# Performance work log

Measured on AMD Instinct MI355X. Metric: run time of the kernel, lower is better.

## Reference

```python
import jax, jax.numpy as jnp
import numpy as np

N, NF1, NF2, NH, OUT, K = 16384, 2000, 10000, 512, 16, 19
BN_EPS = 1e-5

def _bn(x, g, b, m, v):
    # eval-mode BatchNorm1d with running stats
    return (x - m) * jax.lax.rsqrt(v + BN_EPS) * g + b


def setup_inputs() -> dict:
    key = jax.random.key(0)
    ks = jax.random.split(key, 24)
    f32 = jnp.float32
    def w(k, shape):
        return jax.random.normal(k, shape, f32) * 0.02
    inp = {
        "rna": jax.random.normal(ks[0], (N, NF1), f32),
        "atac": jax.random.normal(ks[1], (N, NF2), f32),
        "index_rna": jnp.arange(N, dtype=jnp.int32),
        "index_atac": jnp.arange(N, dtype=jnp.int32),
        "eps": jax.random.normal(ks[2], (N, OUT), f32),
        # RNA encoder
        "W_r1": w(ks[3], (NH, NF1)), "b_r1": jnp.zeros((NH,), f32),
        "g_r": jnp.ones((NH,), f32), "be_r": jnp.zeros((NH,), f32),
        "m_r": jnp.zeros((NH,), f32), "v_r": jnp.ones((NH,), f32),
        "W_rmu": w(ks[4], (OUT, NH)), "b_rmu": jnp.zeros((OUT,), f32),
        "W_rvar": w(ks[5], (OUT, NH)), "b_rvar": jnp.zeros((OUT,), f32),
        # ATAC encoder
        "W_a1": w(ks[6], (NH, NF2)), "b_a1": jnp.zeros((NH,), f32),
        "g_a": jnp.ones((NH,), f32), "be_a": jnp.zeros((NH,), f32),
        "m_a": jnp.zeros((NH,), f32), "v_a": jnp.ones((NH,), f32),
        "W_amu": w(ks[7], (OUT, NH)), "b_amu": jnp.zeros((OUT,), f32),
        "W_avar": w(ks[8], (OUT, NH)), "b_avar": jnp.zeros((OUT,), f32),
        # decoder
        "W_d1": w(ks[9], (NH, OUT)), "b_d1": jnp.zeros((NH,), f32),
        "g_d": jnp.ones((NH,), f32), "be_d": jnp.zeros((NH,), f32),
        "m_d": jnp.zeros((NH,), f32), "v_d": jnp.ones((NH,), f32),
        "W_d4": w(ks[10], (NF1 + NF2, NH)), "b_d4": jnp.zeros((NF1 + NF2,), f32),
        "cluster": jax.random.normal(ks[11], (K, OUT), f32),
    }
    return inp


def reference(rna, atac, index_rna, index_atac, eps,
              W_r1, b_r1, g_r, be_r, m_r, v_r, W_rmu, b_rmu, W_rvar, b_rvar,
              W_a1, b_a1, g_a, be_a, m_a, v_a, W_amu, b_amu, W_avar, b_avar,
              W_d1, b_d1, g_d, be_d, m_d, v_d, W_d4, b_d4, cluster):
    n = rna.shape[0]
    # encoders (dropout is identity in eval mode)
    h_rna = jax.nn.relu(_bn(rna @ W_r1.T + b_r1, g_r, be_r, m_r, v_r))
    zm_rna = h_rna @ W_rmu.T + b_rmu
    zv_rna = jnp.exp(h_rna @ W_rvar.T + b_rvar)
    h_atac = jax.nn.relu(_bn(atac @ W_a1.T + b_a1, g_a, be_a, m_a, v_a))
    zm_atac = h_atac @ W_amu.T + b_amu
    zv_atac = jnp.exp(h_atac @ W_avar.T + b_avar)
    # vectorized scatter replacing the per-sample Python loop
    mu = jnp.ones((n, 2, OUT), rna.dtype)
    var = jnp.ones((n, 2, OUT), rna.dtype)
    mask = jnp.zeros((n, 2, OUT), rna.dtype)
    mu = mu.at[index_rna, 0].set(zm_rna).at[index_atac, 1].set(zm_atac)
    var = var.at[index_rna, 0].set(zv_rna).at[index_atac, 1].set(zv_atac)
    mask = mask.at[index_rna, 0].set(1.0).at[index_atac, 1].set(1.0)
    # product of experts over the modality axis (axis=1)
    T = mask / var
    T_sum = T.sum(axis=1) + 1.0            # [n, OUT]
    z_mu = (mu * T).sum(axis=1) / T_sum
    z_var = 1.0 / T_sum
    # Normal(z_mu, scale=z_var).rsample() with externally supplied eps
    z = z_mu + z_var * eps
    # student-t style soft assignment to clusters
    d2 = jnp.sum((z[:, None, :] - cluster[None, :, :]) ** 2, axis=2)  # [n, K]
    q = 1.0 / (1.0 + d2)
    q = q / q.sum(axis=1, keepdims=True)
    # decoder
    h = jax.nn.relu(_bn(z @ W_d1.T + b_d1, g_d, be_d, m_d, v_d))
    recon_x = h @ W_d4.T + b_d4
    return (recon_x, z_mu, z_var, z, q)
```

## Files before the change

### kernel.cpp

```cpp
#include <hip/hip_runtime.h>
#include <hip/hip_bf16.h>

#define NS    16384
#define NF1c  2000
#define NF2c  10000
#define NH    512
#define KC    19
#define NREC  12000
#define NRECP 12032

typedef short bf16x8 __attribute__((ext_vector_type(8)));
typedef float f32x4  __attribute__((ext_vector_type(4)));

__device__ __forceinline__ unsigned short f2bf(float x) {
    return __builtin_bit_cast(unsigned short, __hip_bfloat16(x));
}
__device__ __forceinline__ float bf2f(unsigned short h) {
    return __builtin_bit_cast(float, (unsigned int)h << 16);
}

__device__ __forceinline__ void sync_nodrain() {
    asm volatile("s_waitcnt lgkmcnt(0)" ::: "memory");
    __builtin_amdgcn_s_barrier();
    asm volatile("" ::: "memory");
}

template<int BK> __device__ __forceinline__ int swz(int r) {
    return (BK == 32) ? ((r >> 1) & 3) : (r & 7);
}

__device__ __forceinline__ void gload16(const unsigned short* g, unsigned short* l) {
    __builtin_amdgcn_global_load_lds(
        (const __attribute__((address_space(1))) void*)g,
        (__attribute__((address_space(3))) void*)l, 16, 0, 0);
}

__global__ void k_cvt(const float* __restrict__ s, unsigned short* __restrict__ d, int n4) {
    int i = blockIdx.x * blockDim.x + threadIdx.x;
    int st = gridDim.x * blockDim.x;
    for (; i < n4; i += st) {
        float4 f = ((const float4*)s)[i];
        ushort4 o;
        o.x = f2bf(f.x); o.y = f2bf(f.y); o.z = f2bf(f.z); o.w = f2bf(f.w);
        ((ushort4*)d)[i] = o;
    }
}

__global__ void k_cvt_pad(const float* __restrict__ s, unsigned short* __restrict__ d,
                          int K, int Rv, long nchunks) {
    long i = (long)blockIdx.x * blockDim.x + threadIdx.x;
    const long stp = (long)gridDim.x * blockDim.x;
    const int Kp8 = K / 8;
    for (; i < nchunks; i += stp) {
        const long row = i / Kp8;
        const int  col = (int)(i - row * Kp8) * 8;
        __align__(16) unsigned short u[8] = {0, 0, 0, 0, 0, 0, 0, 0};
        if (row < Rv) {
            const float* p = s + row * (long)K + col;
            float4 f0 = *(const float4*)p;
            float4 f1 = *(const float4*)(p + 4);
            u[0] = f2bf(f0.x); u[1] = f2bf(f0.y); u[2] = f2bf(f0.z); u[3] = f2bf(f0.w);
            u[4] = f2bf(f1.x); u[5] = f2bf(f1.y); u[6] = f2bf(f1.z); u[7] = f2bf(f1.w);
        }
        *(uint4*)(d + row * (long)K + col) = *(uint4*)u;
    }
}

__global__ void k_prep_st(const float* __restrict__ g, const float* __restrict__ be,
                          const float* __restrict__ m, const float* __restrict__ v,
                          const float* __restrict__ b1,
                          float* __restrict__ s, float* __restrict__ t, int n) {
    int i = blockIdx.x * blockDim.x + threadIdx.x;
    if (i < n) {
        float sc = g[i] * rsqrtf(v[i] + 1e-5f);
        s[i] = sc;
        t[i] = be[i] + (b1[i] - m[i]) * sc;
    }
}

__global__ void k_zero(float* __restrict__ p, int n) {
    int i = blockIdx.x * blockDim.x + threadIdx.x;
    if (i < n) p[i] = 0.f;
}

__global__ __launch_bounds__(256)
void k_gemm(const void* __restrict__ Aptr, const unsigned short* __restrict__ B,
            int K, int Nn, int ntn,
            const float* __restrict__ sc, const float* __restrict__ sh,
            unsigned short* __restrict__ Hout)
{
    constexpr int BK = 64;
    constexpr int JC = BK / 16;
    __shared__ __align__(16) unsigned short As[2][128 * BK];
    __shared__ __align__(16) unsigned short Bs[2][128 * BK];

    const int nwg = gridDim.x;
    const int q8  = nwg >> 3;
    const int L   = (blockIdx.x & 7) * q8 + (blockIdx.x >> 3);
    const int tn  = L % ntn, tm = L / ntn;

    const int tid  = threadIdx.x;
    const int wave = tid >> 6, lane = tid & 63;
    const int wr   = wave >> 1, wc = wave & 1;
    const int lo   = lane & 15, hi = lane >> 4;
    const int srow = tid >> 1, shalf = tid & 1;
    const long arow = (long)tm * 128 + srow;
    const int  brow = tn * 128 + srow;
    const bool bok  = (brow < Nn);

    const float*          Af = (const float*)Aptr + arow * (long)K;
    const unsigned short* Bp = B + (long)brow * K;

    f32x4 acc[4][4];
#pragma unroll
    for (int i = 0; i < 4; i++)
#pragma unroll
        for (int j = 0; j < 4; j++) acc[i][j] = (f32x4){0.f, 0.f, 0.f, 0.f};

    float4 rfa[BK / 8];
    uint4  rb[JC];

    auto issue = [&](int k0, bool tail) {
        const int kb = k0 + shalf * (BK / 2);
        if (!tail) {
#pragma unroll
            for (int q = 0; q < BK / 8; q++) rfa[q] = *(const float4*)(Af + kb + q * 4);
        } else {
#pragma unroll
            for (int q = 0; q < BK / 8; q++) {
                float4 f;
                f.x = (kb + q * 4 + 0 < K) ? Af[kb + q * 4 + 0] : 0.f;
                f.y = (kb + q * 4 + 1 < K) ? Af[kb + q * 4 + 1] : 0.f;
                f.z = (kb + q * 4 + 2 < K) ? Af[kb + q * 4 + 2] : 0.f;
                f.w = (kb + q * 4 + 3 < K) ? Af[kb + q * 4 + 3] : 0.f;
                rfa[q] = f;
            }
        }
#pragma unroll
        for (int j = 0; j < JC; j++) rb[j] = (uint4){0, 0, 0, 0};
        if (bok) {
            if (!tail) {
#pragma unroll
                for (int j = 0; j < JC; j++) rb[j] = *(const uint4*)(Bp + kb + j * 8);
            } else {
#pragma unroll
                for (int j = 0; j < JC; j++) {
                    __align__(16) unsigned short t8[8];
#pragma unroll
                    for (int e = 0; e < 8; e++)
                        t8[e] = (kb + j * 8 + e < K) ? Bp[kb + j * 8 + e] : (unsigned short)0;
                    rb[j] = *(uint4*)t8;
                }
            }
        }
    };

    auto write = [&](int buf) {
        char* Ap = (char*)As[buf];
        char* Bq = (char*)Bs[buf];
        const int rbase = srow * (2 * BK);
        const int sw = swz<BK>(srow);
#pragma unroll
        for (int j = 0; j < JC; j++) {
            const int c = shalf * JC + j;
            const int pos = rbase + ((c ^ sw) << 4);
            uint4 av;
            unsigned int* w32 = (unsigned int*)&av;
            const float* fp = (const float*)&rfa[2 * j];
#pragma unroll
            for (int e = 0; e < 4; e++) {
                unsigned int l16 = f2bf(fp[2 * e]);
                unsigned int h16 = f2bf(fp[2 * e + 1]);
                w32[e] = l16 | (h16 << 16);
            }
            *(uint4*)(Ap + pos) = av;
            *(uint4*)(Bq + pos) = rb[j];
        }
    };

    auto comp = [&](int buf) {
        const char* Ap = (const char*)As[buf];
        const char* Bq = (const char*)Bs[buf];
#pragma unroll
        for (int s = 0; s < BK / 32; s++) {
            bf16x8 af[4], bfv[4];
#pragma unroll
            for (int f = 0; f < 4; f++) {
                const int ar = wr * 64 + f * 16 + lo;
                af[f]  = *(const bf16x8*)(Ap + ar * (2 * BK) + (((s * 4 + hi) ^ swz<BK>(ar)) << 4));
                const int br = wc * 64 + f * 16 + lo;
                bfv[f] = *(const bf16x8*)(Bq + br * (2 * BK) + (((s * 4 + hi) ^ swz<BK>(br)) << 4));
            }
#pragma unroll
            for (int i = 0; i < 4; i++)
#pragma unroll
                for (int j = 0; j < 4; j++)
                    acc[i][j] = __builtin_amdgcn_mfma_f32_16x16x32_bf16(af[i], bfv[j], acc[i][j], 0, 0, 0);
        }
    };

    const int ntf = K / BK;
    const bool rem = (K % BK) != 0;
    const int nt = ntf + (rem ? 1 : 0);
    issue(0, rem && nt == 1);
    for (int t = 0; t < nt; ++t) {
        write(t & 1);
        if (t + 1 < nt) issue((t + 1) * BK, rem && (t + 1 == nt - 1));
        sync_nodrain();
        comp(t & 1);
    }

#pragma unroll
    for (int i = 0; i < 4; i++) {
#pragma unroll
        for (int j = 0; j < 4; j++) {
            const int col = tn * 128 + wc * 64 + j * 16 + lo;
#pragma unroll
            for (int r = 0; r < 4; r++) {
                const long row = (long)tm * 128 + wr * 64 + i * 16 + hi * 4 + r;
                float v = fmaxf(acc[i][j][r] * sc[col] + sh[col], 0.f);
                Hout[row * NH + col] = f2bf(v);
            }
        }
    }
}

__global__ __launch_bounds__(256)
void k_rec(const unsigned short* __restrict__ A, const unsigned short* __restrict__ B,
           const float* __restrict__ bias, float* __restrict__ Fout)
{
    __shared__ __align__(16) unsigned short As[2][128 * 32];
    __shared__ __align__(16) unsigned short Bs[2][128 * 32];

    const int q8 = gridDim.x >> 3;
    const int L  = (blockIdx.x & 7) * q8 + (blockIdx.x >> 3);
    const int tn = L % 94, tm = L / 94;

    const int tid  = threadIdx.x;
    const int wave = tid >> 6, lane = tid & 63;
    const int wr = wave >> 1, wc = wave & 1;
    const int lo = lane & 15, hi = lane >> 4;

    const int rloc = lane >> 2, cch = lane & 3;
    const int row0 = wave * 32 + rloc;
    const int row1 = wave * 32 + 16 + rloc;
    const unsigned short* Ad0 = A + (long)(tm * 128 + row0) * NH + (cch ^ swz<32>(row0)) * 8;
    const unsigned short* Ad1 = A + (long)(tm * 128 + row1) * NH + (cch ^ swz<32>(row1)) * 8;
    const unsigned short* Bd0 = B + (long)(tn * 128 + row0) * NH + (cch ^ swz<32>(row0)) * 8;
    const unsigned short* Bd1 = B + (long)(tn * 128 + row1) * NH + (cch ^ swz<32>(row1)) * 8;

    f32x4 acc[4][4];
#pragma unroll
    for (int i = 0; i < 4; i++)
#pragma unroll
        for (int j = 0; j < 4; j++) acc[i][j] = (f32x4){0.f, 0.f, 0.f, 0.f};

    auto issue = [&](int buf) {
        gload16(Ad0, &As[buf][wave * 1024]);
        gload16(Ad1, &As[buf][wave * 1024 + 512]);
        gload16(Bd0, &Bs[buf][wave * 1024]);
        gload16(Bd1, &Bs[buf][wave * 1024 + 512]);
        Ad0 += 32; Ad1 += 32; Bd0 += 32; Bd1 += 32;
    };
    auto comp = [&](int buf) {
        const char* Ap = (const char*)As[buf];
        const char* Bq = (const char*)Bs[buf];
        bf16x8 af[4], bfv[4];
#pragma unroll
        for (int f = 0; f < 4; f++) {
            const int ar = wr * 64 + f * 16 + lo;
            af[f] = *(const bf16x8*)(Ap + ar * 64 + ((hi ^ swz<32>(ar)) << 4));
            const int br = wc * 64 + f * 16 + lo;
            bfv[f] = *(const bf16x8*)(Bq + br * 64 + ((hi ^ swz<32>(br)) << 4));
        }
        __builtin_amdgcn_s_setprio(1);
#pragma unroll
        for (int i = 0; i < 4; i++)
#pragma unroll
            for (int j = 0; j < 4; j++)
                acc[i][j] = __builtin_amdgcn_mfma_f32_16x16x32_bf16(af[i], bfv[j], acc[i][j], 0, 0, 0);
        __builtin_amdgcn_s_setprio(0);
    };

    const int nt = NH / 32;
    issue(0);
    asm volatile("s_waitcnt vmcnt(0)" ::: "memory");
    __builtin_amdgcn_s_barrier();
    asm volatile("" ::: "memory");

    for (int t = 0; t < nt; ++t) {
        const int c = t & 1;
        const bool more = (t + 1 < nt);
        if (more) issue(c ^ 1);
        comp(c);
        if (more) {
            asm volatile("s_waitcnt vmcnt(0) lgkmcnt(0)" ::: "memory");
            __builtin_amdgcn_s_barrier();
            asm volatile("" ::: "memory");
        }
    }

#pragma unroll
    for (int i = 0; i < 4; i++) {
#pragma unroll
        for (int j = 0; j < 4; j++) {
            const int col = tn * 128 + wc * 64 + j * 16 + lo;
#pragma unroll
            for (int r = 0; r < 4; r++) {
                const long row = (long)tm * 128 + wr * 64 + i * 16 + hi * 4 + r;
                if (col < NREC) Fout[row * (long)NREC + col] = acc[i][j][r] + bias[col];
            }
        }
    }
}

__global__ __launch_bounds__(256)
void k_proj(const unsigned short* __restrict__ h_rna,
            const unsigned short* __restrict__ h_atac,
            const float* __restrict__ W_rmu, const float* __restrict__ b_rmu,
            const float* __restrict__ W_rvar, const float* __restrict__ b_rvar,
            const float* __restrict__ W_amu, const float* __restrict__ b_amu,
            const float* __restrict__ W_avar, const float* __restrict__ b_avar,
            const int* __restrict__ idx_rna, const int* __restrict__ idx_atac,
            float* __restrict__ mu0, float* __restrict__ var0,
            float* __restrict__ mu1, float* __restrict__ var1,
            float* __restrict__ mflag)
{
    __shared__ __align__(16) unsigned short hsh[4][2][NH];
    const int wave = threadIdx.x >> 6, lane = threadIdx.x & 63;
    const long i = (long)blockIdx.x * 4 + wave;
    *(uint4*)&hsh[wave][0][lane * 8] = *(const uint4*)(h_rna  + i * NH + lane * 8);
    *(uint4*)&hsh[wave][1][lane * 8] = *(const uint4*)(h_atac + i * NH + lane * 8);
    __syncthreads();
    const int mod = lane >> 5, oo = lane & 31;
    const int isv = oo >> 4, o = oo & 15;
    const float *W, *bias;
    if (mod == 0) { W = isv ? W_rvar : W_rmu; bias = isv ? b_rvar : b_rmu; }
    else          { W = isv ? W_avar : W_amu; bias = isv ? b_avar : b_amu; }
    const unsigned short* hr = hsh[wave][mod];
    const float* wrow = W + o * NH;
    float a = 0.f;
#pragma unroll 4
    for (int k = 0; k < NH; k += 4) {
        float4 w = *(const float4*)(wrow + k);
        a += bf2f(hr[k]) * w.x + bf2f(hr[k+1]) * w.y + bf2f(hr[k+2]) * w.z + bf2f(hr[k+3]) * w.w;
    }
    a += bias[o];
    const int tgt = (mod == 0) ? idx_rna[i] : idx_atac[i];
    float* mu  = mod ? mu1  : mu0;
    float* var = mod ? var1 : var0;
    if (!isv) mu[(long)tgt * 16 + o] = a;
    else      var[(long)tgt * 16 + o] = expf(a);
    if (oo == 0) mflag[(long)mod * NS + tgt] = 1.f;
}

__global__ __launch_bounds__(256)
void k_combine(const float* __restrict__ mu0, const float* __restrict__ var0,
               const float* __restrict__ mu1, const float* __restrict__ var1,
               const float* __restrict__ mflag,
               const float* __restrict__ eps, const float* __restrict__ cluster,
               const float* __restrict__ W_d1,
               const float* __restrict__ s_d, const float* __restrict__ t_d,
               float* __restrict__ o_zmu, float* __restrict__ o_zvar,
               float* __restrict__ o_z, float* __restrict__ o_q,
               unsigned short* __restrict__ h_d)
{
    __shared__ float zsh[4][16];
    const int wave = threadIdx.x >> 6, lane = threadIdx.x & 63;
    const long i = (long)blockIdx.x * 4 + wave;
    if (lane < 16) {
        const int d = lane;
        const float f0 = mflag[i], f1 = mflag[NS + i];
        float ts = 1.f, num = 0.f;
        if (f0 != 0.f) { float iv = 1.f / var0[i*16+d]; ts += iv; num += mu0[i*16+d] * iv; }
        if (f1 != 0.f) { float iv = 1.f / var1[i*16+d]; ts += iv; num += mu1[i*16+d] * iv; }
        const float zm = num / ts, zv = 1.f / ts;
        const float z = zm + zv * eps[i*16+d];
        o_zmu[i*16+d] = zm; o_zvar[i*16+d] = zv; o_z[i*16+d] = z;
        zsh[wave][d] = z;
    }
    __syncthreads();
    float zreg[16];
#pragma unroll
    for (int d = 0; d < 16; d++) zreg[d] = zsh[wave][d];
    float qk = 0.f;
    if (lane < KC) {
        float d2 = 0.f;
#pragma unroll
        for (int d = 0; d < 16; d++) { float df = zreg[d] - cluster[lane*16+d]; d2 += df*df; }
        qk = 1.f / (1.f + d2);
    }
    float ssum = qk;
#pragma unroll
    for (int off = 16; off > 0; off >>= 1) ssum += __shfl_xor(ssum, off, 32);
    if (lane < KC) o_q[i * KC + lane] = qk / ssum;
#pragma unroll
    for (int j = 0; j < 8; j++) {
        const int c = lane + 64 * j;
        float a = 0.f;
#pragma unroll
        for (int d = 0; d < 16; d += 4) {
            float4 w = *(const float4*)(W_d1 + c * 16 + d);
            a += zreg[d] * w.x + zreg[d+1] * w.y + zreg[d+2] * w.z + zreg[d+3] * w.w;
        }
        a = fmaxf(a * s_d[c] + t_d[c], 0.f);
        h_d[i * NH + c] = f2bf(a);
    }
}

extern "C" void kernel_launch(void* const* d_in, const int* in_sizes, int n_in,
                              void* d_out, int out_size, void* d_ws, size_t ws_size,
                              hipStream_t stream)
{
    const float* rna    = (const float*)d_in[0];
    const float* atac   = (const float*)d_in[1];
    const int*   i_rna  = (const int*)d_in[2];
    const int*   i_atac = (const int*)d_in[3];
    const float* eps    = (const float*)d_in[4];
    const float* W_r1   = (const float*)d_in[5];
    const float* b_r1   = (const float*)d_in[6];
    const float* g_r    = (const float*)d_in[7];
    const float* be_r   = (const float*)d_in[8];
    const float* m_r    = (const float*)d_in[9];
    const float* v_r    = (const float*)d_in[10];
    const float* W_rmu  = (const float*)d_in[11];
    const float* b_rmu  = (const float*)d_in[12];
    const float* W_rvar = (const float*)d_in[13];
    const float* b_rvar = (const float*)d_in[14];
    const float* W_a1   = (const float*)d_in[15];
    const float* b_a1   = (const float*)d_in[16];
    const float* g_a    = (const float*)d_in[17];
    const float* be_a   = (const float*)d_in[18];
    const float* m_a    = (const float*)d_in[19];
    const float* v_a    = (const float*)d_in[20];
    const float* W_amu  = (const float*)d_in[21];
    const float* b_amu  = (const float*)d_in[22];
    const float* W_avar = (const float*)d_in[23];
    const float* b_avar = (const float*)d_in[24];
    const float* W_d1   = (const float*)d_in[25];
    const float* b_d1   = (const float*)d_in[26];
    const float* g_d    = (const float*)d_in[27];
    const float* be_d   = (const float*)d_in[28];
    const float* m_d    = (const float*)d_in[29];
    const float* v_d    = (const float*)d_in[30];
    const float* W_d4   = (const float*)d_in[31];
    const float* b_d4   = (const float*)d_in[32];
    const float* clus   = (const float*)d_in[33];
    (void)in_sizes; (void)n_in; (void)out_size;

    char* w = (char*)d_ws;
    size_t off = 0;
    auto carve = [&](size_t bytes) { void* p = w + off; off += (bytes + 255) & ~(size_t)255; return p; };
    unsigned short* wr1b  = (unsigned short*)carve((size_t)NH * NF1c * 2);
    unsigned short* wa1b  = (unsigned short*)carve((size_t)NH * NF2c * 2);
    unsigned short* wd4b  = (unsigned short*)carve((size_t)NRECP * NH * 2);
    unsigned short* hrna  = (unsigned short*)carve((size_t)NS * NH * 2);
    unsigned short* hatac = (unsigned short*)carve((size_t)NS * NH * 2);
    unsigned short* hd    = (unsigned short*)carve((size_t)NS * NH * 2);
    float* mu0   = (float*)carve((size_t)NS * 16 * 4);
    float* var0  = (float*)carve((size_t)NS * 16 * 4);
    float* mu1   = (float*)carve((size_t)NS * 16 * 4);
    float* var1  = (float*)carve((size_t)NS * 16 * 4);
    float* mflag = (float*)carve((size_t)2 * NS * 4);
    float* st    = (float*)carve((size_t)6 * NH * 4);
    if (off > ws_size) return;

    float* s_r = st;          float* t_r = st + NH;
    float* s_a = st + 2*NH;   float* t_a = st + 3*NH;
    float* s_d = st + 4*NH;   float* t_d = st + 5*NH;

    float* out    = (float*)d_out;
    float* o_rec  = out;
    float* o_zmu  = out + (size_t)NS * NREC;
    float* o_zvar = o_zmu + (size_t)NS * 16;
    float* o_z    = o_zvar + (size_t)NS * 16;
    float* o_q    = o_z + (size_t)NS * 16;

    k_cvt<<<1024, 256, 0, stream>>>(W_r1, wr1b, NH * NF1c / 4);
    k_cvt<<<2048, 256, 0, stream>>>(W_a1, wa1b, NH * NF2c / 4);
    k_cvt_pad<<<2048, 256, 0, stream>>>(W_d4, wd4b, NH, NREC, (long)NRECP * (NH / 8));
    k_prep_st<<<2, 256, 0, stream>>>(g_r, be_r, m_r, v_r, b_r1, s_r, t_r, NH);
    k_prep_st<<<2, 256, 0, stream>>>(g_a, be_a, m_a, v_a, b_a1, s_a, t_a, NH);
    k_prep_st<<<2, 256, 0, stream>>>(g_d, be_d, m_d, v_d, b_d1, s_d, t_d, NH);
    k_zero<<<(2 * NS + 255) / 256, 256, 0, stream>>>(mflag, 2 * NS);

    dim3 blk(256);
    k_gemm<<<512, blk, 0, stream>>>(rna,  wr1b, NF1c, NH, 4, s_r, t_r, hrna);
    k_gemm<<<512, blk, 0, stream>>>(atac, wa1b, NF2c, NH, 4, s_a, t_a, hatac);
    k_proj<<<NS / 4, blk, 0, stream>>>(hrna, hatac, W_rmu, b_rmu, W_rvar, b_rvar,
                                       W_amu, b_amu, W_avar, b_avar, i_rna, i_atac,
                                       mu0, var0, mu1, var1, mflag);
    k_combine<<<NS / 4, blk, 0, stream>>>(mu0, var0, mu1, var1, mflag, eps, clus,
                                          W_d1, s_d, t_d, o_zmu, o_zvar, o_z, o_q, hd);
    k_rec<<<94 * 128, blk, 0, stream>>>(hd, wd4b, b_d4, o_rec);
}
```

Before: 1.225 ms.

## Enlarge decoder output GEMM tile to 256x256 with 8-wave blocks

```diff
diff --git a/kernel.cpp b/kernel.cpp
--- a/kernel.cpp
+++ b/kernel.cpp
@@ -225,90 +225,100 @@
     }
 }
 
-__global__ __launch_bounds__(256)
-void k_rec(const unsigned short* __restrict__ A, const unsigned short* __restrict__ B,
-           const float* __restrict__ bias, float* __restrict__ Fout)
+__global__ __launch_bounds__(512)
+void k_rec256(const unsigned short* __restrict__ A, const unsigned short* __restrict__ B,
+              const float* __restrict__ bias, float* __restrict__ Fout)
 {
-    __shared__ __align__(16) unsigned short As[2][128 * 32];
-    __shared__ __align__(16) unsigned short Bs[2][128 * 32];
+    __shared__ __align__(16) unsigned short As[2][256 * 32];
+    __shared__ __align__(16) unsigned short Bs[2][256 * 32];
 
     const int q8 = gridDim.x >> 3;
     const int L  = (blockIdx.x & 7) * q8 + (blockIdx.x >> 3);
-    const int tn = L % 94, tm = L / 94;
+    const int tn = L % 47, tm = L / 47;
 
     const int tid  = threadIdx.x;
-    const int wave = tid >> 6, lane = tid & 63;
-    const int wr = wave >> 1, wc = wave & 1;
-    const int lo = lane & 15, hi = lane >> 4;
-
-    const int rloc = lane >> 2, cch = lane & 3;
-    const int row0 = wave * 32 + rloc;
-    const int row1 = wave * 32 + 16 + rloc;
-    const unsigned short* Ad0 = A + (long)(tm * 128 + row0) * NH + (cch ^ swz<32>(row0)) * 8;
-    const unsigned short* Ad1 = A + (long)(tm * 128 + row1) * NH + (cch ^ swz<32>(row1)) * 8;
-    const unsigned short* Bd0 = B + (long)(tn * 128 + row0) * NH + (cch ^ swz<32>(row0)) * 8;
-    const unsigned short* Bd1 = B + (long)(tn * 128 + row1) * NH + (cch ^ swz<32>(row1)) * 8;
-
-    f32x4 acc[4][4];
-#pragma unroll
-    for (int i = 0; i < 4; i++)
+    const int w    = tid >> 6, lane = tid & 63;
+    const int wm   = w >> 2, wn = w & 3;
+    const int lo   = lane & 15, hi = lane >> 4;
+
+    const int rl0 = w * 32 + (lane >> 2);
+    const int sch = ((lane & 3) ^ ((lane >> 3) & 3)) * 8;
+    const unsigned short* Adma = A + (size_t)(tm * 256 + rl0) * NH + sch;
+    const unsigned short* Bdma = B + (size_t)(tn * 256 + rl0) * NH + sch;
+
+    f32x4 acc[8][4];
+#pragma unroll
+    for (int i = 0; i < 8; i++)
 #pragma unroll
         for (int j = 0; j < 4; j++) acc[i][j] = (f32x4){0.f, 0.f, 0.f, 0.f};
 
-    auto issue = [&](int buf) {
-        gload16(Ad0, &As[buf][wave * 1024]);
-        gload16(Ad1, &As[buf][wave * 1024 + 512]);
-        gload16(Bd0, &Bs[buf][wave * 1024]);
-        gload16(Bd1, &Bs[buf][wave * 1024 + 512]);
-        Ad0 += 32; Ad1 += 32; Bd0 += 32; Bd1 += 32;
+    auto issue = [&](int buf, int kt) {
+        const int ko = kt * 32;
+        gload16(Adma + ko,            &As[buf][(w * 32) * 32]);
+        gload16(Adma + 16 * NH + ko,  &As[buf][(w * 32 + 16) * 32]);
+        gload16(Bdma + ko,            &Bs[buf][(w * 32) * 32]);
+        gload16(Bdma + 16 * NH + ko,  &Bs[buf][(w * 32 + 16) * 32]);
     };
-    auto comp = [&](int buf) {
-        const char* Ap = (const char*)As[buf];
-        const char* Bq = (const char*)Bs[buf];
-        bf16x8 af[4], bfv[4];
-#pragma unroll
-        for (int f = 0; f < 4; f++) {
-            const int ar = wr * 64 + f * 16 + lo;
-            af[f] = *(const bf16x8*)(Ap + ar * 64 + ((hi ^ swz<32>(ar)) << 4));
-            const int br = wc * 64 + f * 16 + lo;
-            bfv[f] = *(const bf16x8*)(Bq + br * 64 + ((hi ^ swz<32>(br)) << 4));
-        }
-        __builtin_amdgcn_s_setprio(1);
-#pragma unroll
-        for (int i = 0; i < 4; i++)
-#pragma unroll
-            for (int j = 0; j < 4; j++)
-                acc[i][j] = __builtin_amdgcn_mfma_f32_16x16x32_bf16(af[i], bfv[j], acc[i][j], 0, 0, 0);
-        __builtin_amdgcn_s_setprio(0);
+    auto ldA = [&](int buf, int fm) -> bf16x8 {
+        const int ar = wm * 128 + fm * 16 + lo;
+        return *(const bf16x8*)((const char*)As[buf] + ar * 64 + ((hi ^ ((ar >> 1) & 3)) << 4));
     };
+    auto ldB = [&](int buf, int fn) -> bf16x8 {
+        const int br = wn * 64 + fn * 16 + lo;
+        return *(const bf16x8*)((const char*)Bs[buf] + br * 64 + ((hi ^ ((br >> 1) & 3)) << 4));
+    };
 
     const int nt = NH / 32;
-    issue(0);
+    issue(0, 0);
     asm volatile("s_waitcnt vmcnt(0)" ::: "memory");
     __builtin_amdgcn_s_barrier();
     asm volatile("" ::: "memory");
 
-    for (int t = 0; t < nt; ++t) {
-        const int c = t & 1;
-        const bool more = (t + 1 < nt);
-        if (more) issue(c ^ 1);
-        comp(c);
+    for (int kt = 0; kt < nt; ++kt) {
+        const int cur = kt & 1;
+        const bool more = (kt + 1 < nt);
+        if (more) issue(cur ^ 1, kt + 1);
+        bf16x8 bf[4], a0, a1, a2, a3;
+#pragma unroll
+        for (int fn = 0; fn < 4; fn++) bf[fn] = ldB(cur, fn);
+        a0 = ldA(cur, 0); a1 = ldA(cur, 1); a2 = ldA(cur, 2); a3 = ldA(cur, 3);
+        asm volatile("s_waitcnt lgkmcnt(0)" ::: "memory");
+        __builtin_amdgcn_s_setprio(1);
+#pragma unroll
+        for (int fn = 0; fn < 4; fn++) {
+            acc[0][fn] = __builtin_amdgcn_mfma_f32_16x16x32_bf16(a0, bf[fn], acc[0][fn], 0, 0, 0);
+            acc[1][fn] = __builtin_amdgcn_mfma_f32_16x16x32_bf16(a1, bf[fn], acc[1][fn], 0, 0, 0);
+            acc[2][fn] = __builtin_amdgcn_mfma_f32_16x16x32_bf16(a2, bf[fn], acc[2][fn], 0, 0, 0);
+            acc[3][fn] = __builtin_amdgcn_mfma_f32_16x16x32_bf16(a3, bf[fn], acc[3][fn], 0, 0, 0);
+        }
+        __builtin_amdgcn_s_setprio(0);
+        a0 = ldA(cur, 4); a1 = ldA(cur, 5); a2 = ldA(cur, 6); a3 = ldA(cur, 7);
+        asm volatile("s_waitcnt lgkmcnt(0)" ::: "memory");
+        __builtin_amdgcn_s_setprio(1);
+#pragma unroll
+        for (int fn = 0; fn < 4; fn++) {
+            acc[4][fn] = __builtin_amdgcn_mfma_f32_16x16x32_bf16(a0, bf[fn], acc[4][fn], 0, 0, 0);
+            acc[5][fn] = __builtin_amdgcn_mfma_f32_16x16x32_bf16(a1, bf[fn], acc[5][fn], 0, 0, 0);
+            acc[6][fn] = __builtin_amdgcn_mfma_f32_16x16x32_bf16(a2, bf[fn], acc[6][fn], 0, 0, 0);
+            acc[7][fn] = __builtin_amdgcn_mfma_f32_16x16x32_bf16(a3, bf[fn], acc[7][fn], 0, 0, 0);
+        }
+        __builtin_amdgcn_s_setprio(0);
         if (more) {
-            asm volatile("s_waitcnt vmcnt(0) lgkmcnt(0)" ::: "memory");
+            asm volatile("s_waitcnt vmcnt(0)" ::: "memory");
             __builtin_amdgcn_s_barrier();
             asm volatile("" ::: "memory");
         }
     }
 
 #pragma unroll
-    for (int i = 0; i < 4; i++) {
-#pragma unroll
-        for (int j = 0; j < 4; j++) {
-            const int col = tn * 128 + wc * 64 + j * 16 + lo;
+    for (int fm = 0; fm < 8; fm++) {
+#pragma unroll
+        for (int fn = 0; fn < 4; fn++) {
+            const int col = tn * 256 + wn * 64 + fn * 16 + lo;
 #pragma unroll
             for (int r = 0; r < 4; r++) {
-                const long row = (long)tm * 128 + wr * 64 + i * 16 + hi * 4 + r;
-                if (col < NREC) Fout[row * (long)NREC + col] = acc[i][j][r] + bias[col];
+                const long row = (long)tm * 256 + wm * 128 + fm * 16 + hi * 4 + r;
+                if (col < NREC) Fout[row * (long)NREC + col] = acc[fm][fn][r] + bias[col];
             }
         }
     }
@@ -492,5 +502,5 @@
                                        mu0, var0, mu1, var1, mflag);
     k_combine<<<NS / 4, blk, 0, stream>>>(mu0, var0, mu1, var1, mflag, eps, clus,
                                           W_d1, s_d, t_d, o_zmu, o_zvar, o_z, o_q, hd);
-    k_rec<<<94 * 128, blk, 0, stream>>>(hd, wd4b, b_d4, o_rec);
-}
+    k_rec256<<<3008, dim3(512), 0, stream>>>(hd, wd4b, b_d4, o_rec);
+}
```

After: 1.201 ms. About the same (-1.9%).
